# Performance work log

Hardware: AMD Instinct MI355X
Metric: run time of the kernel (lower is better)

The kernel has to match this reference:

```python
import jax, jax.numpy as jnp
import numpy as np

N_NODES, N_EDGES = 1600, 32000
C = 128            # sphere_channels
LMAX, MMAX = 6, 2
M0 = LMAX + 1      # number of m=0 coefficients (7)
N_SPH = (LMAX + 1) ** 2   # 49 full harmonics after inverse Wigner rotation
BASIS = 512        # distance expansion size
MAX_ELEM = 90
HID = 128
RESCALE = 23.395238876342773


def _build_to_m(lmax, mmax):
    # CoefficientMappingModule.to_m: permutation from l-primary to m-primary order
    m_c = []
    for l in range(lmax + 1):
        mm = min(mmax, l)
        m_c.extend(range(-mm, mm + 1))
    m_c = np.array(m_c)
    n = len(m_c)
    to_m = np.zeros((n, n), np.float32)
    off = 0
    for m in range(mmax + 1):
        idx_r = np.nonzero(m_c == m)[0]
        for o, i in enumerate(idx_r):
            to_m[o + off, i] = 1.0
        off += len(idx_r)
        if m > 0:
            idx_i = np.nonzero(m_c == -m)[0]
            for o, i in enumerate(idx_i):
                to_m[o + off, i] = 1.0
            off += len(idx_i)
    return to_m

_TO_M = _build_to_m(LMAX, MMAX)
N_ALL = _TO_M.shape[0]   # 29


def setup_inputs() -> dict:
    key = jax.random.key(0)
    ks = jax.random.split(key, 12)
    d_in = BASIS + 2 * HID   # 768 (distance basis + source/target atom embeddings)
    return {
        "atomic_numbers": jax.random.randint(ks[0], (N_NODES,), 0, MAX_ELEM),
        "edge_distance": jax.random.uniform(ks[1], (N_EDGES, BASIS), dtype=jnp.float32),
        "edge_index": jax.random.randint(ks[2], (2, N_EDGES), 0, N_NODES),
        "src_table": jax.random.uniform(ks[3], (MAX_ELEM, HID), minval=-0.001, maxval=0.001),
        "tgt_table": jax.random.uniform(ks[4], (MAX_ELEM, HID), minval=-0.001, maxval=0.001),
        "w1": jax.random.normal(ks[5], (d_in, HID)) / np.float32(np.sqrt(d_in)),
        "b1": jnp.zeros((HID,), jnp.float32),
        "g1": jnp.ones((HID,), jnp.float32),
        "be1": jnp.zeros((HID,), jnp.float32),
        "w2": jax.random.normal(ks[6], (HID, HID)) / np.float32(np.sqrt(HID)),
        "b2": jnp.zeros((HID,), jnp.float32),
        "g2": jnp.ones((HID,), jnp.float32),
        "be2": jnp.zeros((HID,), jnp.float32),
        "w3": jax.random.normal(ks[7], (HID, M0 * C)) / np.float32(np.sqrt(HID)),
        "b3": jnp.zeros((M0 * C,), jnp.float32),
        "to_m": jnp.asarray(_TO_M),
        "wigner_inv": jax.random.normal(ks[8], (N_EDGES, N_SPH, N_ALL)) * 0.2,
    }


def _ln(x, g, b, eps=1e-5):
    mu = jnp.mean(x, axis=-1, keepdims=True)
    var = jnp.var(x, axis=-1, keepdims=True)
    return (x - mu) * jax.lax.rsqrt(var + eps) * g + b


def reference(atomic_numbers, edge_distance, edge_index, src_table, tgt_table,
              w1, b1, g1, be1, w2, b2, g2, be2, w3, b3, to_m, wigner_inv):
    E = edge_distance.shape[0]
    # atom-edge embedding gathers
    src = src_table[atomic_numbers[edge_index[0]]]            # [E, HID]
    tgt = tgt_table[atomic_numbers[edge_index[1]]]            # [E, HID]
    x = jnp.concatenate([edge_distance, src, tgt], axis=1)    # [E, 768]
    # RadialFunction: Linear -> LN -> SiLU -> Linear -> LN -> SiLU -> Linear
    h = jax.nn.silu(_ln(x @ w1 + b1, g1, be1))
    h = jax.nn.silu(_ln(h @ w2 + b2, g2, be2))
    x0 = (h @ w3 + b3).reshape(E, M0, C)                      # m=0 coefficients
    # _l_primary: to_m.T @ emb. Padded rows (m != 0) are zero, so only the
    # first M0 rows of to_m contribute.
    x_l = jnp.einsum("emc,ml->elc", x0, to_m[:M0])            # [E, N_ALL, C]
    # _rotate_inv: per-edge inverse Wigner-D rotation to full harmonics
    x_rot = jnp.einsum("eij,ejc->eic", wigner_inv, x_l)       # [E, N_SPH, C]
    # _reduce_edge: scatter-add onto target nodes, then rescale
    out = jax.ops.segment_sum(x_rot, edge_index[1], num_segments=N_NODES)
    return out / RESCALE
```

## Files before the change

kernel.cpp:

```cpp
#include <hip/hip_runtime.h>
#include <hip/hip_bf16.h>

#define NE 32000
#define NNODES 1600
#define CCH 128
#define M0C 7
#define NSPH 49
#define NALLC 29
#define BASIS 512
#define DIN 768
#define HID 128
#define RESCALE_F 23.395238876342773f
#define CH 28
#define MAXCH (NE / CH + NNODES)
#define WCROW 8
#define WCPE (NSPH * WCROW)
#define WC_OFF 82558976ull
#define WC_BYTES (2ull * NE * WCPE)

typedef __bf16 bf16x8 __attribute__((ext_vector_type(8)));
typedef __bf16 bf16x2 __attribute__((ext_vector_type(2)));
typedef float  f32x4  __attribute__((ext_vector_type(4)));

__device__ __forceinline__ unsigned short f_to_bf16(float f) {
    unsigned int u = __float_as_uint(f);
    unsigned int r = (u + 0x7FFFu + ((u >> 16) & 1u)) >> 16;
    return (unsigned short)r;
}
__device__ __forceinline__ float silu_f(float x) {
    return x / (1.0f + __expf(-x));
}

__global__ __launch_bounds__(256) void prepack_w(
    const float* __restrict__ w1, const float* __restrict__ w2, const float* __restrict__ w3,
    unsigned short* __restrict__ w1p,
    unsigned short* __restrict__ w2p,
    unsigned short* __restrict__ w3p)
{
    int idx = blockIdx.x * 256 + threadIdx.x;
    if (idx < 98304) {
        int kstep = idx >> 12;
        int ct    = (idx >> 9) & 7;
        int li    = idx & 511;
        int lane = li >> 3, j = li & 7;
        int m = lane & 15, quad = lane >> 4;
        int k = kstep * 32 + quad * 8 + j;
        int n = ct * 16 + m;
        w1p[idx] = f_to_bf16(w1[(size_t)k * 128 + n]);
    } else if (idx < 114688) {
        int j2 = idx - 98304;
        int kstep = j2 >> 12;
        int ct    = (j2 >> 9) & 7;
        int li    = j2 & 511;
        int lane = li >> 3, j = li & 7;
        int m = lane & 15, quad = lane >> 4;
        int k = kstep * 32 + quad * 8 + j;
        int n = ct * 16 + m;
        w2p[j2] = f_to_bf16(w2[(size_t)k * 128 + n]);
    } else if (idx < 229376) {
        int j3 = idx - 114688;
        int kstep = j3 / 28672;
        int r     = j3 - kstep * 28672;
        int o     = r >> 12;
        int ctile = (r >> 9) & 7;
        int li    = r & 511;
        int lane = li >> 3, j = li & 7;
        int m = lane & 15, quad = lane >> 4;
        int k = kstep * 32 + quad * 8 + j;
        int n = o * 128 + ctile * 16 + m;
        w3p[j3] = f_to_bf16(w3[(size_t)k * 896 + n]);
    }
}

__global__ __launch_bounds__(256) void gemm1_ln_mfma(
    const float* __restrict__ dist,
    const int* __restrict__ edge_index,
    const int* __restrict__ atomic_numbers,
    const float* __restrict__ src_table,
    const float* __restrict__ tgt_table,
    const unsigned short* __restrict__ w1p,
    const float* __restrict__ bias,
    const float* __restrict__ gam,
    const float* __restrict__ bet,
    unsigned short* __restrict__ Out)
{
    __shared__ unsigned short Ad[64][512];

    const int t = threadIdx.x;
    const int wv = t >> 6, lane = t & 63;
    const int m = lane & 15, quad = lane >> 4;
    const int row0 = blockIdx.x * 64;

    {
        const float4* src = (const float4*)(dist + (size_t)row0 * 512);
#pragma unroll 8
        for (int it = 0; it < 32; ++it) {
            int u = it * 256 + t;
            float4 v = src[u];
            int row = u >> 7;
            int c4  = (u & 127) * 4;
            int gs  = (c4 >> 3) ^ (row & 7);
            unsigned short* d = &Ad[row][gs * 8 + (c4 & 7)];
            d[0] = f_to_bf16(v.x); d[1] = f_to_bf16(v.y);
            d[2] = f_to_bf16(v.z); d[3] = f_to_bf16(v.w);
        }
    }

    const int arow = wv * 16 + m;
    const int row  = row0 + arow;
    const int sid  = atomic_numbers[edge_index[row]];
    const int tid2 = atomic_numbers[edge_index[NE + row]];
    const float* a1 = src_table + sid * 128 + quad * 8;
    const float* a2 = tgt_table + tid2 * 128 + quad * 8;
    const unsigned short* bb = w1p + lane * 8;
    __syncthreads();

    f32x4 acc[8] = {};

#pragma unroll
    for (int k0 = 0; k0 < 768; k0 += 32) {
        bf16x8 af;
        if (k0 < 512) {
            int gs = ((k0 >> 3) + quad) ^ (arow & 7);
            af = *(const bf16x8*)&Ad[arow][gs * 8];
        } else {
            const float* ap = (k0 < 640) ? (a1 + (k0 - 512)) : (a2 + (k0 - 640));
            float4 va = *(const float4*)ap;
            float4 vb = *(const float4*)(ap + 4);
            af[0] = (__bf16)va.x; af[1] = (__bf16)va.y;
            af[2] = (__bf16)va.z; af[3] = (__bf16)va.w;
            af[4] = (__bf16)vb.x; af[5] = (__bf16)vb.y;
            af[6] = (__bf16)vb.z; af[7] = (__bf16)vb.w;
        }
#pragma unroll
        for (int ct = 0; ct < 8; ++ct) {
            bf16x8 bfv = *(const bf16x8*)(bb + (size_t)(((k0 >> 5) * 8 + ct)) * 512);
            acc[ct] = __builtin_amdgcn_mfma_f32_16x16x32_bf16(af, bfv, acc[ct], 0, 0, 0);
        }
    }

    float bbv[8], ggv[8], eev[8];
#pragma unroll
    for (int ct = 0; ct < 8; ++ct) {
        bbv[ct] = bias[ct * 16 + m];
        ggv[ct] = gam[ct * 16 + m];
        eev[ct] = bet[ct * 16 + m];
    }
#pragma unroll
    for (int reg = 0; reg < 4; ++reg) {
        float v[8];
        float s = 0.f, s2 = 0.f;
#pragma unroll
        for (int ct = 0; ct < 8; ++ct) {
            v[ct] = acc[ct][reg] + bbv[ct];
            s += v[ct]; s2 += v[ct] * v[ct];
        }
#pragma unroll
        for (int off = 1; off < 16; off <<= 1) {
            s  += __shfl_xor(s, off, 64);
            s2 += __shfl_xor(s2, off, 64);
        }
        float mean = s * (1.0f / 128.0f);
        float var  = s2 * (1.0f / 128.0f) - mean * mean;
        float rstd = rsqrtf(var + 1e-5f);
        int orow = row0 + wv * 16 + 4 * quad + reg;
#pragma unroll
        for (int ct = 0; ct < 8; ++ct) {
            float o = silu_f((v[ct] - mean) * rstd * ggv[ct] + eev[ct]);
            Out[(size_t)orow * 128 + ct * 16 + m] = f_to_bf16(o);
        }
    }
}

__global__ __launch_bounds__(256) void gemm2_ln_mfma(
    const unsigned short* __restrict__ A,
    const unsigned short* __restrict__ w2p,
    const float* __restrict__ bias,
    const float* __restrict__ gam,
    const float* __restrict__ bet,
    unsigned short* __restrict__ Out)
{
    const int t = threadIdx.x;
    const int wv = t >> 6, lane = t & 63;
    const int m = lane & 15, quad = lane >> 4;
    const int row0 = blockIdx.x * 64 + wv * 16;

    f32x4 acc[8] = {};
    const unsigned short* arow = A + (size_t)(row0 + m) * 128 + quad * 8;
    const unsigned short* bb   = w2p + lane * 8;

#pragma unroll
    for (int k0 = 0; k0 < 128; k0 += 32) {
        bf16x8 af = *(const bf16x8*)(arow + k0);
#pragma unroll
        for (int ct = 0; ct < 8; ++ct) {
            bf16x8 bfv = *(const bf16x8*)(bb + (size_t)(((k0 >> 5) * 8 + ct)) * 512);
            acc[ct] = __builtin_amdgcn_mfma_f32_16x16x32_bf16(af, bfv, acc[ct], 0, 0, 0);
        }
    }

    float bbv[8], ggv[8], eev[8];
#pragma unroll
    for (int ct = 0; ct < 8; ++ct) {
        bbv[ct] = bias[ct * 16 + m];
        ggv[ct] = gam[ct * 16 + m];
        eev[ct] = bet[ct * 16 + m];
    }
#pragma unroll
    for (int reg = 0; reg < 4; ++reg) {
        float v[8];
        float s = 0.f, s2 = 0.f;
#pragma unroll
        for (int ct = 0; ct < 8; ++ct) {
            v[ct] = acc[ct][reg] + bbv[ct];
            s += v[ct]; s2 += v[ct] * v[ct];
        }
#pragma unroll
        for (int off = 1; off < 16; off <<= 1) {
            s  += __shfl_xor(s, off, 64);
            s2 += __shfl_xor(s2, off, 64);
        }
        float mean = s * (1.0f / 128.0f);
        float var  = s2 * (1.0f / 128.0f) - mean * mean;
        float rstd = rsqrtf(var + 1e-5f);
        int row = row0 + 4 * quad + reg;
#pragma unroll
        for (int ct = 0; ct < 8; ++ct) {
            float o = silu_f((v[ct] - mean) * rstd * ggv[ct] + eev[ct]);
            Out[(size_t)row * 128 + ct * 16 + m] = f_to_bf16(o);
        }
    }
}

__global__ __launch_bounds__(256) void gemm3_mfma(
    const unsigned short* __restrict__ A,
    const unsigned short* __restrict__ w3p,
    const float* __restrict__ b3,
    unsigned short* __restrict__ X0p)
{
    const int t = threadIdx.x;
    const int wv = t >> 6, lane = t & 63;
    const int m = lane & 15, quad = lane >> 4;
    const int row0 = blockIdx.x * 16;
    const int c0 = wv * 32;

    f32x4 acc[14] = {};
    const unsigned short* arow = A + (size_t)(row0 + m) * 128 + quad * 8;
    const unsigned short* bb   = w3p + lane * 8;

#pragma unroll
    for (int k0 = 0; k0 < 128; k0 += 32) {
        bf16x8 af = *(const bf16x8*)(arow + k0);
#pragma unroll
        for (int o = 0; o < 7; ++o) {
#pragma unroll
            for (int ch2 = 0; ch2 < 2; ++ch2) {
                bf16x8 bfv = *(const bf16x8*)(bb +
                    (size_t)((((k0 >> 5) * 7 + o) * 8 + (wv * 2 + ch2))) * 512);
                acc[o * 2 + ch2] =
                    __builtin_amdgcn_mfma_f32_16x16x32_bf16(af, bfv, acc[o * 2 + ch2], 0, 0, 0);
            }
        }
    }

    const float inv_res = 1.0f / RESCALE_F;
    float bv[14];
#pragma unroll
    for (int o = 0; o < 7; ++o)
#pragma unroll
        for (int ch2 = 0; ch2 < 2; ++ch2)
            bv[o * 2 + ch2] = b3[o * 128 + c0 + ch2 * 16 + m];

#pragma unroll
    for (int reg = 0; reg < 4; ++reg) {
        int row = row0 + 4 * quad + reg;
#pragma unroll
        for (int ch2 = 0; ch2 < 2; ++ch2) {
            int c = c0 + ch2 * 16 + m;
            union { unsigned short us[8]; uint4 q; } pk;
#pragma unroll
            for (int o = 0; o < 7; ++o)
                pk.us[o] = f_to_bf16((acc[o * 2 + ch2][reg] + bv[o * 2 + ch2]) * inv_res);
            pk.us[7] = 0;
            *(uint4*)(X0p + (size_t)row * 1024 + c * 8) = pk.q;
        }
    }
}

__global__ __launch_bounds__(256) void hist_kernel(
    const int* __restrict__ edge_index, int* __restrict__ cnt)
{
    int e = blockIdx.x * 256 + threadIdx.x;
    if (e < NE) atomicAdd(&cnt[edge_index[NE + e]], 1);
}

__global__ __launch_bounds__(256) void scan_kernel(
    const int* __restrict__ cnt, int* __restrict__ offs, int* __restrict__ cur)
{
    __shared__ int part[256];
    const int t = threadIdx.x;
    const int base = t * 7;
    int s = 0;
#pragma unroll
    for (int j = 0; j < 7; ++j) {
        int i = base + j;
        if (i < NNODES) s += cnt[i];
    }
    part[t] = s;
    __syncthreads();
    for (int off = 1; off < 256; off <<= 1) {
        int v = (t >= off) ? part[t - off] : 0;
        __syncthreads();
        part[t] += v;
        __syncthreads();
    }
    int run = (t > 0) ? part[t - 1] : 0;
#pragma unroll
    for (int j = 0; j < 7; ++j) {
        int i = base + j;
        if (i < NNODES) {
            offs[i] = run;
            cur[i] = run;
            run += cnt[i];
        }
    }
    if (t == 0) offs[NNODES] = part[255];
}

__global__ __launch_bounds__(256) void scatter_kernel(
    const int* __restrict__ edge_index, int* __restrict__ cur, int* __restrict__ order)
{
    int e = blockIdx.x * 256 + threadIdx.x;
    if (e < NE) {
        int tgt = edge_index[NE + e];
        int pos = atomicAdd(&cur[tgt], 1);
        order[pos] = e;
    }
}

__global__ __launch_bounds__(256) void build_chunks(
    const int* __restrict__ offs, int* __restrict__ chunk_cnt,
    int* __restrict__ ch_node, int* __restrict__ ch_beg, int* __restrict__ ch_lm)
{
    int n = blockIdx.x * 256 + threadIdx.x;
    if (n >= NNODES) return;
    int b = offs[n], k = offs[n + 1] - b;
    if (k == 0) return;
    int nc = (k + CH - 1) / CH;
    int base = atomicAdd(chunk_cnt, nc);
    for (int c = 0; c < nc; ++c) {
        ch_node[base + c] = n;
        ch_beg[base + c]  = b + CH * c;
        int l = min(CH, k - CH * c);
        ch_lm[base + c] = l | ((nc > 1) ? 0x10000 : 0);
    }
}

__global__ __launch_bounds__(256) void wig_extract(
    const float* __restrict__ wig,
    const int* __restrict__ order,
    unsigned short* __restrict__ Wc)
{
    __shared__ float raw[8 * 1421];
    __shared__ int eloc[8];

    const int t = threadIdx.x;
    const int p0 = blockIdx.x * 8;
    if (t < 8) eloc[t] = order[p0 + t];
    __syncthreads();

    {
        const int g = t >> 5, l = t & 31;
        const float* src = wig + (size_t)eloc[g] * (NSPH * NALLC);
        float* dst = raw + g * 1421;
#pragma unroll
        for (int it = 0; it < 45; ++it) {
            int i = it * 32 + l;
            if (i < 1421) dst[i] = src[i];
        }
    }
    __syncthreads();

    uint4* wout = (uint4*)(Wc + (size_t)p0 * WCPE);
    for (int q = t; q < 8 * NSPH; q += 256) {
        int pl = q / NSPH, row = q - pl * NSPH;
        const float* r = raw + pl * 1421 + row * NALLC;
        union { unsigned short us[8]; uint4 v; } pk;
        pk.us[0] = f_to_bf16(r[0]);
        pk.us[1] = f_to_bf16(r[2]);
        pk.us[2] = f_to_bf16(r[6]);
        pk.us[3] = f_to_bf16(r[11]);
        pk.us[4] = f_to_bf16(r[16]);
        pk.us[5] = f_to_bf16(r[21]);
        pk.us[6] = f_to_bf16(r[26]);
        pk.us[7] = 0;
        wout[q] = pk.v;
    }
}

__global__ __launch_bounds__(256) void rotate_chunks_mfma(
    const unsigned short* __restrict__ X0p,
    const float* __restrict__ wig,
    const unsigned short* __restrict__ Wc,
    const int use_wc,
    const int* __restrict__ order,
    const int* __restrict__ chunk_cnt,
    const int* __restrict__ ch_node,
    const int* __restrict__ ch_beg,
    const int* __restrict__ ch_lm,
    float* __restrict__ out)
{
    __shared__ unsigned short Ws[CH][64][8];
    __shared__ int es[CH];

    const int b = blockIdx.x;
    if (b >= chunk_cnt[0]) return;
    const int node = ch_node[b];
    const int beg  = ch_beg[b];
    const int lm   = ch_lm[b];
    const int len  = lm & 0xFFFF;
    const int multi = lm >> 16;

    const int t = threadIdx.x;
    const int wv = t >> 6, lane = t & 63;
    const int m = lane & 15, quad = lane >> 4;

    if (t < CH) es[t] = order[beg + ((t < len) ? t : 0)];

    if (use_wc) {
        const uint4* wsrc = (const uint4*)(Wc + (size_t)beg * WCPE);
        const int nval = len * NSPH;
        for (int q = t; q < CH * NSPH; q += 256) {
            int slot = q / NSPH, row = q - slot * NSPH;
            uint4 v = make_uint4(0u, 0u, 0u, 0u);
            if (q < nval) v = wsrc[q];
            *(uint4*)&Ws[slot][row][0] = v;
        }
        for (int q = t; q < CH * 15; q += 256) {
            int slot = q / 15, row = 49 + (q - (q / 15) * 15);
            *(uint4*)&Ws[slot][row][0] = make_uint4(0u, 0u, 0u, 0u);
        }
    } else {
        const int slot8 = t >> 3;
        const int lane8 = t & 7;
        if (slot8 < CH) {
            const int e = (slot8 < len) ? order[beg + slot8] : -1;
            const float* wsrc = wig + (size_t)e * (NSPH * NALLC);
#pragma unroll
            for (int j = 0; j < 49; ++j) {
                int idx = j * 8 + lane8;
                int i = idx >> 3, o = idx & 7;
                float v = 0.f;
                if (e >= 0 && o < 7) {
                    int col = (o < 2) ? (2 * o) : (5 * o - 4);
                    v = wsrc[i * NALLC + col];
                }
                Ws[slot8][i][o] = f_to_bf16(v);
            }
#pragma unroll
            for (int j = 0; j < 15; ++j)
                Ws[slot8][49 + j][lane8] = 0;
        }
    }
    __syncthreads();

    f32x4 acc[8] = {};
    for (int g = 0; g < 7; ++g) {
        const int e = es[g * 4 + quad];
        const unsigned short* xb = X0p + (size_t)e * 1024 + m * 8;
        bf16x8 aq = *(const bf16x8*)&Ws[g * 4 + quad][wv * 16 + m][0];
#pragma unroll
        for (int nt = 0; nt < 8; ++nt) {
            bf16x8 bq = *(const bf16x8*)(xb + nt * 128);
            acc[nt] = __builtin_amdgcn_mfma_f32_16x16x32_bf16(aq, bq, acc[nt], 0, 0, 0);
        }
    }

    float* op = out + (size_t)node * (NSPH * CCH);
    const int r0 = wv * 16 + quad * 4;
    if (multi) {
#pragma unroll
        for (int nt = 0; nt < 8; ++nt) {
            int c = nt * 16 + m;
#pragma unroll
            for (int reg = 0; reg < 4; ++reg) {
                int sph = r0 + reg;
                if (sph < NSPH) atomicAdd(&op[sph * CCH + c], acc[nt][reg]);
            }
        }
    } else {
#pragma unroll
        for (int nt = 0; nt < 8; ++nt) {
            int c = nt * 16 + m;
#pragma unroll
            for (int reg = 0; reg < 4; ++reg) {
                int sph = r0 + reg;
                if (sph < NSPH) op[sph * CCH + c] = acc[nt][reg];
            }
        }
    }
}

extern "C" void kernel_launch(void* const* d_in, const int* in_sizes, int n_in,
                              void* d_out, int out_size, void* d_ws, size_t ws_size,
                              hipStream_t stream) {
    const int*   atomic_numbers = (const int*)d_in[0];
    const float* edge_distance  = (const float*)d_in[1];
    const int*   edge_index     = (const int*)d_in[2];
    const float* src_table      = (const float*)d_in[3];
    const float* tgt_table      = (const float*)d_in[4];
    const float* w1  = (const float*)d_in[5];
    const float* b1  = (const float*)d_in[6];
    const float* g1  = (const float*)d_in[7];
    const float* be1 = (const float*)d_in[8];
    const float* w2  = (const float*)d_in[9];
    const float* b2  = (const float*)d_in[10];
    const float* g2  = (const float*)d_in[11];
    const float* be2 = (const float*)d_in[12];
    const float* w3  = (const float*)d_in[13];
    const float* b3  = (const float*)d_in[14];
    const float* wig = (const float*)d_in[16];

    char* ws = (char*)d_ws;
    unsigned short* H1b = (unsigned short*)(ws);
    unsigned short* H2b = (unsigned short*)(ws + 8192000);
    unsigned short* X0p = (unsigned short*)(ws + 16384000);
    unsigned short* w1p = (unsigned short*)(ws + 81920000);
    unsigned short* w2p = (unsigned short*)(ws + 82116608);
    unsigned short* w3p = (unsigned short*)(ws + 82149376);
    int* ints      = (int*)(ws + 82378752);
    int* cnt       = ints;
    int* chunk_cnt = cnt + NNODES;
    int* offs      = chunk_cnt + 1;
    int* cur       = offs + NNODES + 1;
    int* order     = cur + NNODES;
    int* ch_node   = order + NE;
    int* ch_beg    = ch_node + MAXCH;
    int* ch_lm     = ch_beg + MAXCH;
    const int use_wc = (ws_size >= WC_OFF + WC_BYTES) ? 1 : 0;
    unsigned short* Wc = (unsigned short*)(ws + WC_OFF);

    hipMemsetAsync(cnt, 0, (NNODES + 1) * sizeof(int), stream);
    hipMemsetAsync(d_out, 0, (size_t)out_size * sizeof(float), stream);

    hist_kernel<<<(NE + 255) / 256, 256, 0, stream>>>(edge_index, cnt);
    scan_kernel<<<1, 256, 0, stream>>>(cnt, offs, cur);
    scatter_kernel<<<(NE + 255) / 256, 256, 0, stream>>>(edge_index, cur, order);
    build_chunks<<<(NNODES + 255) / 256, 256, 0, stream>>>(
        offs, chunk_cnt, ch_node, ch_beg, ch_lm);

    if (use_wc)
        wig_extract<<<NE / 8, 256, 0, stream>>>(wig, order, Wc);

    prepack_w<<<(229376 + 255) / 256, 256, 0, stream>>>(w1, w2, w3, w1p, w2p, w3p);
    gemm1_ln_mfma<<<NE / 64, 256, 0, stream>>>(
        edge_distance, edge_index, atomic_numbers, src_table, tgt_table,
        w1p, b1, g1, be1, H1b);
    gemm2_ln_mfma<<<NE / 64, 256, 0, stream>>>(H1b, w2p, b2, g2, be2, H2b);
    gemm3_mfma<<<NE / 16, 256, 0, stream>>>(H2b, w3p, b3, X0p);

    rotate_chunks_mfma<<<MAXCH, 256, 0, stream>>>(
        X0p, wig, Wc, use_wc, order, chunk_cnt, ch_node, ch_beg, ch_lm,
        (float*)d_out);
}
```

Measured before the change: 465.1 us.

## Load GEMM1 distance tile directly from global and skip empty chunk slots

The first GEMM kernel no longer stages the 64x512 distance tile into shared memory. Each lane now reads its fp32 A fragment straight from global memory and converts it to bf16 in registers, which removes the LDS staging, the swizzle and the barrier but gives up coalesced tile loads. The scatter kernel now bounds its Wigner loading, zero-fill and MFMA loop by the actual chunk length rounded up to a group of 4, so partially filled chunks skip padded work.

```diff
diff --git a/kernel.cpp b/kernel.cpp
--- a/kernel.cpp
+++ b/kernel.cpp
@@ -84,54 +84,33 @@
     const float* __restrict__ bet,
     unsigned short* __restrict__ Out)
 {
-    __shared__ unsigned short Ad[64][512];
-
     const int t = threadIdx.x;
     const int wv = t >> 6, lane = t & 63;
     const int m = lane & 15, quad = lane >> 4;
-    const int row0 = blockIdx.x * 64;
-
-    {
-        const float4* src = (const float4*)(dist + (size_t)row0 * 512);
-#pragma unroll 8
-        for (int it = 0; it < 32; ++it) {
-            int u = it * 256 + t;
-            float4 v = src[u];
-            int row = u >> 7;
-            int c4  = (u & 127) * 4;
-            int gs  = (c4 >> 3) ^ (row & 7);
-            unsigned short* d = &Ad[row][gs * 8 + (c4 & 7)];
-            d[0] = f_to_bf16(v.x); d[1] = f_to_bf16(v.y);
-            d[2] = f_to_bf16(v.z); d[3] = f_to_bf16(v.w);
-        }
-    }
-
-    const int arow = wv * 16 + m;
-    const int row  = row0 + arow;
+    const int row0 = blockIdx.x * 64 + wv * 16;
+    const int row = row0 + m;
+
     const int sid  = atomic_numbers[edge_index[row]];
     const int tid2 = atomic_numbers[edge_index[NE + row]];
+    const float* a0 = dist + (size_t)row * 512 + quad * 8;
     const float* a1 = src_table + sid * 128 + quad * 8;
     const float* a2 = tgt_table + tid2 * 128 + quad * 8;
     const unsigned short* bb = w1p + lane * 8;
-    __syncthreads();
 
     f32x4 acc[8] = {};
 
 #pragma unroll
     for (int k0 = 0; k0 < 768; k0 += 32) {
+        const float* ap = (k0 < 512) ? (a0 + k0)
+                        : (k0 < 640) ? (a1 + (k0 - 512))
+                                     : (a2 + (k0 - 640));
+        float4 va = *(const float4*)ap;
+        float4 vb = *(const float4*)(ap + 4);
         bf16x8 af;
-        if (k0 < 512) {
-            int gs = ((k0 >> 3) + quad) ^ (arow & 7);
-            af = *(const bf16x8*)&Ad[arow][gs * 8];
-        } else {
-            const float* ap = (k0 < 640) ? (a1 + (k0 - 512)) : (a2 + (k0 - 640));
-            float4 va = *(const float4*)ap;
-            float4 vb = *(const float4*)(ap + 4);
-            af[0] = (__bf16)va.x; af[1] = (__bf16)va.y;
-            af[2] = (__bf16)va.z; af[3] = (__bf16)va.w;
-            af[4] = (__bf16)vb.x; af[5] = (__bf16)vb.y;
-            af[6] = (__bf16)vb.z; af[7] = (__bf16)vb.w;
-        }
+        af[0] = (__bf16)va.x; af[1] = (__bf16)va.y;
+        af[2] = (__bf16)va.z; af[3] = (__bf16)va.w;
+        af[4] = (__bf16)vb.x; af[5] = (__bf16)vb.y;
+        af[6] = (__bf16)vb.z; af[7] = (__bf16)vb.w;
 #pragma unroll
         for (int ct = 0; ct < 8; ++ct) {
             bf16x8 bfv = *(const bf16x8*)(bb + (size_t)(((k0 >> 5) * 8 + ct)) * 512);
@@ -163,7 +142,7 @@
         float mean = s * (1.0f / 128.0f);
         float var  = s2 * (1.0f / 128.0f) - mean * mean;
         float rstd = rsqrtf(var + 1e-5f);
-        int orow = row0 + wv * 16 + 4 * quad + reg;
+        int orow = row0 + 4 * quad + reg;
 #pragma unroll
         for (int ct = 0; ct < 8; ++ct) {
             float o = silu_f((v[ct] - mean) * rstd * ggv[ct] + eev[ct]);
@@ -420,6 +399,8 @@
     const int lm   = ch_lm[b];
     const int len  = lm & 0xFFFF;
     const int multi = lm >> 16;
+    const int gmax  = (len + 3) >> 2;
+    const int nslot = gmax * 4;
 
     const int t = threadIdx.x;
     const int wv = t >> 6, lane = t & 63;
@@ -430,20 +411,20 @@
     if (use_wc) {
         const uint4* wsrc = (const uint4*)(Wc + (size_t)beg * WCPE);
         const int nval = len * NSPH;
-        for (int q = t; q < CH * NSPH; q += 256) {
+        for (int q = t; q < nslot * NSPH; q += 256) {
             int slot = q / NSPH, row = q - slot * NSPH;
             uint4 v = make_uint4(0u, 0u, 0u, 0u);
             if (q < nval) v = wsrc[q];
             *(uint4*)&Ws[slot][row][0] = v;
         }
-        for (int q = t; q < CH * 15; q += 256) {
+        for (int q = t; q < nslot * 15; q += 256) {
             int slot = q / 15, row = 49 + (q - (q / 15) * 15);
             *(uint4*)&Ws[slot][row][0] = make_uint4(0u, 0u, 0u, 0u);
         }
     } else {
         const int slot8 = t >> 3;
         const int lane8 = t & 7;
-        if (slot8 < CH) {
+        if (slot8 < nslot) {
             const int e = (slot8 < len) ? order[beg + slot8] : -1;
             const float* wsrc = wig + (size_t)e * (NSPH * NALLC);
 #pragma unroll
@@ -465,7 +446,7 @@
     __syncthreads();
 
     f32x4 acc[8] = {};
-    for (int g = 0; g < 7; ++g) {
+    for (int g = 0; g < gmax; ++g) {
         const int e = es[g * 4 + quad];
         const unsigned short* xb = X0p + (size_t)e * 1024 + m * 8;
         bf16x8 aq = *(const bf16x8*)&Ws[g * 4 + quad][wv * 16 + m][0];
```

New measurement: 456.6 us. No clear change (-1.8%).
